# Kernel optimization log

Hardware: AMD Instinct MI355X
Metric: run time of the kernel (lower is better)

## Reference

```python
import jax, jax.numpy as jnp
import numpy as np

N_HEAD = 16


def setup_inputs() -> dict:
    key = jax.random.key(0)
    ks = jax.random.split(key, 4)
    B, T, C = 4, 2048, 1024
    x = jax.random.normal(ks[0], (B, T, C), dtype=jnp.float32)
    w_qkv = jax.random.normal(ks[1], (C, 3 * C), dtype=jnp.float32) * (1.0 / np.sqrt(C))
    b_qkv = jnp.zeros((3 * C,), dtype=jnp.float32)
    w_out = jax.random.normal(ks[2], (C, C), dtype=jnp.float32) * (1.0 / np.sqrt(C))
    b_out = jnp.zeros((C,), dtype=jnp.float32)
    return {"x": x, "w_qkv": w_qkv, "b_qkv": b_qkv, "w_out": w_out, "b_out": b_out}


def reference(x, w_qkv, b_qkv, w_out, b_out):
    B, T, C = x.shape
    H = N_HEAD
    D = C // H  # head_dim
    qkv = x @ w_qkv + b_qkv                      # [B,T,3C]
    q, k, v = jnp.split(qkv, 3, axis=-1)
    # [B,T,C] -> [B,H,T,D]
    q = q.reshape(B, T, H, D).transpose(0, 2, 1, 3)
    k = k.reshape(B, T, H, D).transpose(0, 2, 1, 3)
    v = v.reshape(B, T, H, D).transpose(0, 2, 1, 3)
    scores = jnp.einsum('bhqd,bhkd->bhqk', q, k) / jnp.sqrt(jnp.float32(D))
    causal = jnp.tril(jnp.ones((T, T), dtype=bool))
    scores = jnp.where(causal, scores, jnp.float32(-jnp.inf))
    attn = jax.nn.softmax(scores, axis=-1)       # dropout omitted (eval, p=0)
    out = jnp.einsum('bhqk,bhkd->bhqd', attn, v)
    out = out.transpose(0, 2, 1, 3).reshape(B, T, C)
    out = out @ w_out + b_out
    return out
```

## Files before the change

kernel.cpp:

```cpp
#include <hip/hip_runtime.h>
#include <hip/hip_bf16.h>

typedef unsigned short u16;
typedef unsigned int u32;
typedef __attribute__((ext_vector_type(8))) __bf16 bhalf8;
typedef __attribute__((ext_vector_type(8))) u16 us8;
typedef __attribute__((ext_vector_type(4))) u16 us4;
typedef __attribute__((ext_vector_type(4))) float f32x4;

#if __has_builtin(__builtin_amdgcn_mfma_f32_16x16x16_bf16)
typedef __attribute__((ext_vector_type(4))) __bf16 bhalf4;
#define MFMA16(a, b, c) __builtin_amdgcn_mfma_f32_16x16x16_bf16(a, b, c, 0, 0, 0)
#else
typedef __attribute__((ext_vector_type(4))) short bhalf4;
#define MFMA16(a, b, c) __builtin_amdgcn_mfma_f32_16x16x16bf16_1k(a, b, c, 0, 0, 0)
#endif

#if __has_builtin(__builtin_amdgcn_exp2f)
#define EXP2(x) __builtin_amdgcn_exp2f(x)
#else
#define EXP2(x) exp2f(x)
#endif

__device__ __forceinline__ u16 bf16rne(float f) {
  u32 u = __float_as_uint(f);
  u += 0x7FFFu + ((u >> 16) & 1u);
  return (u16)(u >> 16);
}

__device__ __forceinline__ u32 pkbf(float a, float b) {
  union { __hip_bfloat162 h; u32 w; } u;
  u.h = __float22bfloat162_rn(make_float2(a, b));
  return u.w;
}

__global__ __launch_bounds__(256) void cast4_kernel(const float* __restrict__ in,
                                                    u16* __restrict__ out, int n) {
  int i = (blockIdx.x * 256 + threadIdx.x) * 4;
  if (i >= n) return;
  float4 f = *(const float4*)(in + i);
  u32 lo = pkbf(f.x, f.y);
  u32 hi = pkbf(f.z, f.w);
  *(uint2*)(out + i) = make_uint2(lo, hi);
}

__global__ __launch_bounds__(256) void transpose_cast_kernel(const float* __restrict__ in,
                                                             u16* __restrict__ out,
                                                             int R, int Cn) {
  __shared__ float tile[32][33];
  int c0 = blockIdx.x * 32, r0 = blockIdx.y * 32;
  int tx = threadIdx.x, ty = threadIdx.y;
#pragma unroll
  for (int j = 0; j < 4; ++j)
    tile[ty + j * 8][tx] = in[(size_t)(r0 + ty + j * 8) * Cn + c0 + tx];
  __syncthreads();
#pragma unroll
  for (int j = 0; j < 4; ++j)
    out[(size_t)(c0 + ty + j * 8) * R + r0 + tx] = bf16rne(tile[tx][ty + j * 8]);
}

template <int MODE>
__global__ __launch_bounds__(256, 2) void gemm_bt_kernel(
    const u16* __restrict__ A, const u16* __restrict__ Bt, const float* __restrict__ bias,
    float* __restrict__ outf, u16* __restrict__ qb, u16* __restrict__ kb, u16* __restrict__ vb,
    int Mdim, int Ndim, int Kdim) {
  __shared__ __align__(16) u16 lA[128 * 64];
  __shared__ __align__(16) u16 lB[128 * 64];
  const int tid = threadIdx.x;
  const int lane = tid & 63;
  const int col = lane & 15, quad = lane >> 4;
  const int wid = tid >> 6;
  const int gx = (MODE == 0) ? 24 : 8;
  int id = blockIdx.y * gx + blockIdx.x;
  int g = id & 7, j = id >> 3;
  int vy = g * 8 + j / gx;
  int vx = j % gx;
  const int m0 = vy * 128, n0 = vx * 128;
  const int wm = (wid >> 1) * 64, wn = (wid & 1) * 64;
  const float QSC = 0.18033688011112042f;

  f32x4 acc[4][4];
#pragma unroll
  for (int i = 0; i < 4; ++i)
#pragma unroll
    for (int j2 = 0; j2 < 4; ++j2) acc[i][j2] = f32x4{0.f, 0.f, 0.f, 0.f};

  for (int k0 = 0; k0 < Kdim; k0 += 64) {
    const u16* Ag = A + (size_t)m0 * Kdim + k0;
    const u16* Bg = Bt + (size_t)n0 * Kdim + k0;
#pragma unroll
    for (int r = 0; r < 4; ++r) {
      int c = r * 256 + tid;
      int row = c >> 3;
      int bblk = (c & 7) ^ (row & 7);
      size_t ldsoff = (size_t)(r * 256 + (tid & 0xC0)) * 8;
      __builtin_amdgcn_global_load_lds(
          (const __attribute__((address_space(1))) void*)(Ag + (size_t)row * Kdim + bblk * 8),
          (__attribute__((address_space(3))) void*)(lA + ldsoff), 16, 0, 0);
      __builtin_amdgcn_global_load_lds(
          (const __attribute__((address_space(1))) void*)(Bg + (size_t)row * Kdim + bblk * 8),
          (__attribute__((address_space(3))) void*)(lB + ldsoff), 16, 0, 0);
    }
    __syncthreads();
#pragma unroll
    for (int ks = 0; ks < 2; ++ks) {
      bhalf8 af[4], bfr[4];
#pragma unroll
      for (int i = 0; i < 4; ++i) {
        int ra = wm + i * 16 + col;
        int rb = wn + i * 16 + col;
        af[i]  = *(const bhalf8*)&lA[ra * 64 + (((ks * 4 + quad) ^ (ra & 7)) * 8)];
        bfr[i] = *(const bhalf8*)&lB[rb * 64 + (((ks * 4 + quad) ^ (rb & 7)) * 8)];
      }
#pragma unroll
      for (int mt = 0; mt < 4; ++mt)
#pragma unroll
        for (int nt = 0; nt < 4; ++nt)
          acc[mt][nt] = __builtin_amdgcn_mfma_f32_16x16x32_bf16(af[mt], bfr[nt], acc[mt][nt], 0, 0, 0);
    }
    __syncthreads();
  }

  if (MODE == 0) {
#pragma unroll
    for (int nt = 0; nt < 4; ++nt) {
      int n = n0 + wn + nt * 16 + col;
      float bv = bias[n];
      int which = n >> 10, cc = n & 1023, hh = cc >> 6, dd = cc & 63;
      if (which == 2) {
#pragma unroll
        for (int mt = 0; mt < 4; ++mt) {
          int t0 = m0 + wm + mt * 16 + quad * 4;
          int bb = t0 >> 11, tt = t0 & 2047;
          us4 w;
#pragma unroll
          for (int reg = 0; reg < 4; ++reg) w[reg] = bf16rne(acc[mt][nt][reg] + bv);
          *(us4*)(vb + ((size_t)(bb * 16 + hh) * 64 + dd) * 2048 + tt) = w;
        }
      } else {
        u16* dst = which ? kb : qb;
        float sc = which ? 1.0f : QSC;
#pragma unroll
        for (int mt = 0; mt < 4; ++mt)
#pragma unroll
          for (int reg = 0; reg < 4; ++reg) {
            int m = m0 + wm + mt * 16 + quad * 4 + reg;
            int bb = m >> 11, tt = m & 2047;
            dst[((size_t)(bb * 16 + hh) * 2048 + tt) * 64 + dd] = bf16rne((acc[mt][nt][reg] + bv) * sc);
          }
      }
    }
  } else {
#pragma unroll
    for (int mt = 0; mt < 4; ++mt)
#pragma unroll
      for (int nt = 0; nt < 4; ++nt) {
        int n = n0 + wn + nt * 16 + col;
        float bv = bias[n];
#pragma unroll
        for (int reg = 0; reg < 4; ++reg) {
          int m = m0 + wm + mt * 16 + quad * 4 + reg;
          outf[(size_t)m * Ndim + n] = acc[mt][nt][reg] + bv;
        }
      }
  }
}

__global__ __launch_bounds__(256, 2) void attn_kernel(const u16* __restrict__ Q,
                                                      const u16* __restrict__ K,
                                                      const u16* __restrict__ VT,
                                                      u16* __restrict__ aout) {
  __shared__ __align__(16) u16 lK[2][128 * 64];
  __shared__ __align__(16) u16 lV[2][64 * 128];
  const int tid = threadIdx.x;
  const int lane = tid & 63, wid = tid >> 6;
  const int col = lane & 15, quad = lane >> 4;
  int id = blockIdx.y * 8 + blockIdx.x;
  int g = id & 7, j = id >> 3;
  const int bh = g * 8 + (j >> 3);
  const int bx = j & 7;
  const int b = bh >> 4, h = bh & 15;
  const u16* Qb = Q + (size_t)bh * 2048 * 64;
  const u16* Kb = K + (size_t)bh * 2048 * 64;
  const u16* Vb = VT + (size_t)bh * 64 * 2048;
  const int qbase = wid * 32;
  const int wuni = (tid & 0xC0);

  for (int phase = 0; phase < 2; ++phase) {
    const int qt = (phase == 0) ? (15 - bx) : bx;

    auto stage = [&](int kt, int bufi) {
      const u16* Kg = Kb + (size_t)kt * 128 * 64;
      const u16* Vg = Vb + (size_t)kt * 128;
#pragma unroll
      for (int r = 0; r < 4; ++r) {
        int c = r * 256 + tid;
        size_t ldsoff = (size_t)(r * 256 + wuni) * 8;
        int krow = c >> 3, kblk = (c & 7) ^ (krow & 7);
        __builtin_amdgcn_global_load_lds(
            (const __attribute__((address_space(1))) void*)(Kg + (size_t)krow * 64 + kblk * 8),
            (__attribute__((address_space(3))) void*)(&lK[bufi][0] + ldsoff), 16, 0, 0);
        int vrow = c >> 4, vblk = (c & 15) ^ (vrow & 15);
        __builtin_amdgcn_global_load_lds(
            (const __attribute__((address_space(1))) void*)(Vg + (size_t)vrow * 2048 + vblk * 8),
            (__attribute__((address_space(3))) void*)(&lV[bufi][0] + ldsoff), 16, 0, 0);
      }
    };

    bhalf8 qf[2][2];
#pragma unroll
    for (int ntq = 0; ntq < 2; ++ntq)
#pragma unroll
      for (int ks = 0; ks < 2; ++ks)
        qf[ntq][ks] = *(const bhalf8*)(Qb + (size_t)(qt * 128 + qbase + ntq * 16 + col) * 64 +
                                       ks * 32 + quad * 8);

    f32x4 oacc[4][2];
    float lr[2] = {0.f, 0.f};
#pragma unroll
    for (int dt = 0; dt < 4; ++dt)
#pragma unroll
      for (int ntq = 0; ntq < 2; ++ntq) oacc[dt][ntq] = f32x4{0.f, 0.f, 0.f, 0.f};

    stage(0, 0);

    for (int kt = 0; kt <= qt; ++kt) {
      const int cur = kt & 1;
      __syncthreads();
      if (kt < qt) stage(kt + 1, cur ^ 1);
      const bool diag = (kt == qt);
      const int ntkhi = diag ? (2 * wid + 2) : 8;

      f32x4 sacc[8][2];
#pragma unroll
      for (int ntk = 0; ntk < 8; ++ntk)
#pragma unroll
        for (int ntq = 0; ntq < 2; ++ntq) sacc[ntk][ntq] = f32x4{0.f, 0.f, 0.f, 0.f};
#pragma unroll
      for (int ks = 0; ks < 2; ++ks) {
        bhalf8 kf[8];
#pragma unroll
        for (int ntk = 0; ntk < 8; ++ntk)
          if (ntk < ntkhi) {
            int ra = ntk * 16 + col;
            kf[ntk] = *(const bhalf8*)&lK[cur][ra * 64 + (((ks * 4 + quad) ^ (ra & 7)) * 8)];
          }
#pragma unroll
        for (int ntk = 0; ntk < 8; ++ntk)
          if (ntk < ntkhi) {
#pragma unroll
            for (int ntq = 0; ntq < 2; ++ntq)
              sacc[ntk][ntq] = __builtin_amdgcn_mfma_f32_16x16x32_bf16(kf[ntk], qf[ntq][ks],
                                                                       sacc[ntk][ntq], 0, 0, 0);
          }
      }

      if (diag) {
#pragma unroll
        for (int ntk = 0; ntk < 8; ++ntk)
          if (ntk >= 2 * wid && ntk < 2 * wid + 2) {
#pragma unroll
            for (int ntq = 0; ntq < 2; ++ntq) {
              int qloc = qbase + ntq * 16 + col;
#pragma unroll
              for (int reg = 0; reg < 4; ++reg) {
                int kloc = ntk * 16 + quad * 4 + reg;
                if (kloc > qloc) sacc[ntk][ntq][reg] = -1e30f;
              }
            }
          }
      }

#pragma unroll
      for (int ntk = 0; ntk < 8; ++ntk)
        if (ntk < ntkhi) {
          bhalf4 vf[4];
#pragma unroll
          for (int dt = 0; dt < 4; ++dt) {
            int vrow = dt * 16 + col;
            vf[dt] = *(const bhalf4*)&lV[cur][vrow * 128 +
                                             (((ntk * 2 + (quad >> 1)) ^ col) * 8) + (quad & 1) * 4];
          }
#pragma unroll
          for (int ntq = 0; ntq < 2; ++ntq) {
            float p0 = EXP2(sacc[ntk][ntq][0]);
            float p1 = EXP2(sacc[ntk][ntq][1]);
            float p2 = EXP2(sacc[ntk][ntq][2]);
            float p3 = EXP2(sacc[ntk][ntq][3]);
            lr[ntq] += (p0 + p1) + (p2 + p3);
            union { u32 w[2]; bhalf4 v; } pfu;
            pfu.w[0] = pkbf(p0, p1);
            pfu.w[1] = pkbf(p2, p3);
#pragma unroll
            for (int dt = 0; dt < 4; ++dt)
              oacc[dt][ntq] = MFMA16(vf[dt], pfu.v, oacc[dt][ntq]);
          }
        }
    }

#pragma unroll
    for (int ntq = 0; ntq < 2; ++ntq) {
      float r = lr[ntq];
      r += __shfl_xor(r, 16);
      r += __shfl_xor(r, 32);
      float inv = 1.f / r;
      int q = qt * 128 + qbase + ntq * 16 + col;
      size_t base = ((size_t)(b * 2048 + q)) * 1024 + h * 64;
#pragma unroll
      for (int dt = 0; dt < 4; ++dt) {
        us4 w;
#pragma unroll
        for (int reg = 0; reg < 4; ++reg) w[reg] = bf16rne(oacc[dt][ntq][reg] * inv);
        *(us4*)(aout + base + dt * 16 + quad * 4) = w;
      }
    }
    __syncthreads();
  }
}

extern "C" void kernel_launch(void* const* d_in, const int* in_sizes, int n_in,
                              void* d_out, int out_size, void* d_ws, size_t ws_size,
                              hipStream_t stream) {
  const float* x     = (const float*)d_in[0];
  const float* w_qkv = (const float*)d_in[1];
  const float* b_qkv = (const float*)d_in[2];
  const float* w_out = (const float*)d_in[3];
  const float* b_out = (const float*)d_in[4];
  float* out = (float*)d_out;
  char* ws = (char*)d_ws;
  u16* xb    = (u16*)(ws);
  u16* wqkvT = (u16*)(ws + 16777216);
  u16* woutT = (u16*)(ws + 23068672);
  u16* qb    = (u16*)(ws + 25165824);
  u16* kb    = (u16*)(ws + 41943040);
  u16* vT    = (u16*)(ws + 58720256);
  u16* ab    = (u16*)(ws + 75497472);

  cast4_kernel<<<8192, 256, 0, stream>>>(x, xb, 8388608);
  dim3 tb(32, 8);
  transpose_cast_kernel<<<dim3(96, 32), tb, 0, stream>>>(w_qkv, wqkvT, 1024, 3072);
  transpose_cast_kernel<<<dim3(32, 32), tb, 0, stream>>>(w_out, woutT, 1024, 1024);
  gemm_bt_kernel<0><<<dim3(24, 64), 256, 0, stream>>>(xb, wqkvT, b_qkv, nullptr, qb, kb, vT,
                                                      8192, 3072, 1024);
  attn_kernel<<<dim3(8, 64), 256, 0, stream>>>(qb, kb, vT, ab);
  gemm_bt_kernel<1><<<dim3(8, 64), 256, 0, stream>>>(ab, woutT, b_out, out, nullptr, nullptr,
                                                     nullptr, 8192, 1024, 1024);
}
```

Measured before the change: 245.8 us.

## Shrink attention K/V tiles to 64 keys and merge prep kernels

```diff
diff --git a/kernel.cpp b/kernel.cpp
--- a/kernel.cpp
+++ b/kernel.cpp
@@ -34,22 +34,10 @@
   return u.w;
 }
 
-__global__ __launch_bounds__(256) void cast4_kernel(const float* __restrict__ in,
-                                                    u16* __restrict__ out, int n) {
-  int i = (blockIdx.x * 256 + threadIdx.x) * 4;
-  if (i >= n) return;
-  float4 f = *(const float4*)(in + i);
-  u32 lo = pkbf(f.x, f.y);
-  u32 hi = pkbf(f.z, f.w);
-  *(uint2*)(out + i) = make_uint2(lo, hi);
-}
-
-__global__ __launch_bounds__(256) void transpose_cast_kernel(const float* __restrict__ in,
-                                                             u16* __restrict__ out,
-                                                             int R, int Cn) {
+__device__ __forceinline__ void tcast_tile(const float* __restrict__ in, u16* __restrict__ out,
+                                           int R, int Cn, int c0, int r0, int tid) {
   __shared__ float tile[32][33];
-  int c0 = blockIdx.x * 32, r0 = blockIdx.y * 32;
-  int tx = threadIdx.x, ty = threadIdx.y;
+  int tx = tid & 31, ty = tid >> 5;
 #pragma unroll
   for (int j = 0; j < 4; ++j)
     tile[ty + j * 8][tx] = in[(size_t)(r0 + ty + j * 8) * Cn + c0 + tx];
@@ -57,6 +45,26 @@
 #pragma unroll
   for (int j = 0; j < 4; ++j)
     out[(size_t)(c0 + ty + j * 8) * R + r0 + tx] = bf16rne(tile[tx][ty + j * 8]);
+}
+
+__global__ __launch_bounds__(256) void prep_kernel(const float* __restrict__ x,
+                                                   const float* __restrict__ wqkv,
+                                                   const float* __restrict__ wout,
+                                                   u16* __restrict__ xb,
+                                                   u16* __restrict__ wqkvT,
+                                                   u16* __restrict__ woutT) {
+  int bid = blockIdx.x, tid = threadIdx.x;
+  if (bid < 8192) {
+    int i = (bid * 256 + tid) * 4;
+    float4 f = *(const float4*)(x + i);
+    *(uint2*)(xb + i) = make_uint2(pkbf(f.x, f.y), pkbf(f.z, f.w));
+  } else if (bid < 11264) {
+    int t = bid - 8192;
+    tcast_tile(wqkv, wqkvT, 1024, 3072, (t % 96) * 32, (t / 96) * 32, tid);
+  } else {
+    int t = bid - 11264;
+    tcast_tile(wout, woutT, 1024, 1024, (t % 32) * 32, (t / 32) * 32, tid);
+  }
 }
 
 template <int MODE>
@@ -166,12 +174,12 @@
   }
 }
 
-__global__ __launch_bounds__(256, 2) void attn_kernel(const u16* __restrict__ Q,
+__global__ __launch_bounds__(256, 4) void attn_kernel(const u16* __restrict__ Q,
                                                       const u16* __restrict__ K,
                                                       const u16* __restrict__ VT,
                                                       u16* __restrict__ aout) {
-  __shared__ __align__(16) u16 lK[2][128 * 64];
-  __shared__ __align__(16) u16 lV[2][64 * 128];
+  __shared__ __align__(16) u16 lK[2][64 * 64];
+  __shared__ __align__(16) u16 lV[2][64 * 64];
   const int tid = threadIdx.x;
   const int lane = tid & 63, wid = tid >> 6;
   const int col = lane & 15, quad = lane >> 4;
@@ -183,26 +191,31 @@
   const u16* Qb = Q + (size_t)bh * 2048 * 64;
   const u16* Kb = K + (size_t)bh * 2048 * 64;
   const u16* Vb = VT + (size_t)bh * 64 * 2048;
-  const int qbase = wid * 32;
-  const int wuni = (tid & 0xC0);
+  const int wuni = tid & 0xC0;
+
+  const int loffK0 = col * 64 + ((quad ^ (col & 7)) * 8);
+  const int loffK1 = col * 64 + (((4 + quad) ^ (col & 7)) * 8);
+  int loffV[4];
+#pragma unroll
+  for (int ntk = 0; ntk < 4; ++ntk)
+    loffV[ntk] = col * 64 + (((ntk * 2 + (quad >> 1)) ^ (col & 7)) * 8) + (quad & 1) * 4;
 
   for (int phase = 0; phase < 2; ++phase) {
     const int qt = (phase == 0) ? (15 - bx) : bx;
 
     auto stage = [&](int kt, int bufi) {
-      const u16* Kg = Kb + (size_t)kt * 128 * 64;
-      const u16* Vg = Vb + (size_t)kt * 128;
-#pragma unroll
-      for (int r = 0; r < 4; ++r) {
+      const u16* Kg = Kb + (size_t)kt * 64 * 64;
+      const u16* Vg = Vb + (size_t)kt * 64;
+#pragma unroll
+      for (int r = 0; r < 2; ++r) {
         int c = r * 256 + tid;
         size_t ldsoff = (size_t)(r * 256 + wuni) * 8;
-        int krow = c >> 3, kblk = (c & 7) ^ (krow & 7);
+        int row = c >> 3, blk = (c & 7) ^ (row & 7);
         __builtin_amdgcn_global_load_lds(
-            (const __attribute__((address_space(1))) void*)(Kg + (size_t)krow * 64 + kblk * 8),
+            (const __attribute__((address_space(1))) void*)(Kg + (size_t)row * 64 + blk * 8),
             (__attribute__((address_space(3))) void*)(&lK[bufi][0] + ldsoff), 16, 0, 0);
-        int vrow = c >> 4, vblk = (c & 15) ^ (vrow & 15);
         __builtin_amdgcn_global_load_lds(
-            (const __attribute__((address_space(1))) void*)(Vg + (size_t)vrow * 2048 + vblk * 8),
+            (const __attribute__((address_space(1))) void*)(Vg + (size_t)row * 2048 + blk * 8),
             (__attribute__((address_space(3))) void*)(&lV[bufi][0] + ldsoff), 16, 0, 0);
       }
     };
@@ -212,7 +225,7 @@
     for (int ntq = 0; ntq < 2; ++ntq)
 #pragma unroll
       for (int ks = 0; ks < 2; ++ks)
-        qf[ntq][ks] = *(const bhalf8*)(Qb + (size_t)(qt * 128 + qbase + ntq * 16 + col) * 64 +
+        qf[ntq][ks] = *(const bhalf8*)(Qb + (size_t)(qt * 128 + wid * 32 + ntq * 16 + col) * 64 +
                                        ks * 32 + quad * 8);
 
     f32x4 oacc[4][2];
@@ -222,65 +235,90 @@
 #pragma unroll
       for (int ntq = 0; ntq < 2; ++ntq) oacc[dt][ntq] = f32x4{0.f, 0.f, 0.f, 0.f};
 
-    stage(0, 0);
-
-    for (int kt = 0; kt <= qt; ++kt) {
-      const int cur = kt & 1;
-      __syncthreads();
-      if (kt < qt) stage(kt + 1, cur ^ 1);
-      const bool diag = (kt == qt);
-      const int ntkhi = diag ? (2 * wid + 2) : 8;
-
-      f32x4 sacc[8][2];
-#pragma unroll
-      for (int ntk = 0; ntk < 8; ++ntk)
+    auto compute_full = [&](const u16* Kbuf, const u16* Vbuf) {
+      f32x4 sacc[4][2];
+#pragma unroll
+      for (int ntk = 0; ntk < 4; ++ntk)
 #pragma unroll
         for (int ntq = 0; ntq < 2; ++ntq) sacc[ntk][ntq] = f32x4{0.f, 0.f, 0.f, 0.f};
 #pragma unroll
       for (int ks = 0; ks < 2; ++ks) {
-        bhalf8 kf[8];
-#pragma unroll
-        for (int ntk = 0; ntk < 8; ++ntk)
-          if (ntk < ntkhi) {
-            int ra = ntk * 16 + col;
-            kf[ntk] = *(const bhalf8*)&lK[cur][ra * 64 + (((ks * 4 + quad) ^ (ra & 7)) * 8)];
-          }
-#pragma unroll
-        for (int ntk = 0; ntk < 8; ++ntk)
-          if (ntk < ntkhi) {
+        const int lk = ks ? loffK1 : loffK0;
+        bhalf8 kf[4];
+#pragma unroll
+        for (int ntk = 0; ntk < 4; ++ntk) kf[ntk] = *(const bhalf8*)(Kbuf + lk + ntk * 1024);
+#pragma unroll
+        for (int ntk = 0; ntk < 4; ++ntk)
+#pragma unroll
+          for (int ntq = 0; ntq < 2; ++ntq)
+            sacc[ntk][ntq] = __builtin_amdgcn_mfma_f32_16x16x32_bf16(kf[ntk], qf[ntq][ks],
+                                                                     sacc[ntk][ntq], 0, 0, 0);
+      }
+#pragma unroll
+      for (int ntk = 0; ntk < 4; ++ntk) {
+        bhalf4 vf[4];
+#pragma unroll
+        for (int dt = 0; dt < 4; ++dt)
+          vf[dt] = *(const bhalf4*)(Vbuf + loffV[ntk] + dt * 1024);
+#pragma unroll
+        for (int ntq = 0; ntq < 2; ++ntq) {
+          float p0 = EXP2(sacc[ntk][ntq][0]);
+          float p1 = EXP2(sacc[ntk][ntq][1]);
+          float p2 = EXP2(sacc[ntk][ntq][2]);
+          float p3 = EXP2(sacc[ntk][ntq][3]);
+          lr[ntq] += (p0 + p1) + (p2 + p3);
+          union { u32 w[2]; bhalf4 v; } pfu;
+          pfu.w[0] = pkbf(p0, p1);
+          pfu.w[1] = pkbf(p2, p3);
+#pragma unroll
+          for (int dt = 0; dt < 4; ++dt)
+            oacc[dt][ntq] = MFMA16(vf[dt], pfu.v, oacc[dt][ntq]);
+        }
+      }
+    };
+
+    auto compute_diag = [&](const u16* Kbuf, const u16* Vbuf, int kbase) {
+      const int ntkhi = (wid & 1) ? 4 : 2;
+      const int ntklo = (wid & 1) * 2;
+      f32x4 sacc[4][2];
+#pragma unroll
+      for (int ntk = 0; ntk < 4; ++ntk)
+#pragma unroll
+        for (int ntq = 0; ntq < 2; ++ntq) sacc[ntk][ntq] = f32x4{0.f, 0.f, 0.f, 0.f};
+#pragma unroll
+      for (int ks = 0; ks < 2; ++ks) {
+        const int lk = ks ? loffK1 : loffK0;
+        bhalf8 kf[4];
+#pragma unroll
+        for (int ntk = 0; ntk < 4; ++ntk)
+          if (ntk < ntkhi) kf[ntk] = *(const bhalf8*)(Kbuf + lk + ntk * 1024);
+#pragma unroll
+        for (int ntk = 0; ntk < 4; ++ntk)
+          if (ntk < ntkhi)
 #pragma unroll
             for (int ntq = 0; ntq < 2; ++ntq)
               sacc[ntk][ntq] = __builtin_amdgcn_mfma_f32_16x16x32_bf16(kf[ntk], qf[ntq][ks],
                                                                        sacc[ntk][ntq], 0, 0, 0);
-          }
-      }
-
-      if (diag) {
-#pragma unroll
-        for (int ntk = 0; ntk < 8; ++ntk)
-          if (ntk >= 2 * wid && ntk < 2 * wid + 2) {
-#pragma unroll
-            for (int ntq = 0; ntq < 2; ++ntq) {
-              int qloc = qbase + ntq * 16 + col;
-#pragma unroll
-              for (int reg = 0; reg < 4; ++reg) {
-                int kloc = ntk * 16 + quad * 4 + reg;
-                if (kloc > qloc) sacc[ntk][ntq][reg] = -1e30f;
-              }
+      }
+#pragma unroll
+      for (int ntk = 0; ntk < 4; ++ntk)
+        if (ntk >= ntklo && ntk < ntkhi)
+#pragma unroll
+          for (int ntq = 0; ntq < 2; ++ntq) {
+            int qloc = wid * 32 + ntq * 16 + col;
+#pragma unroll
+            for (int reg = 0; reg < 4; ++reg) {
+              int kloc = kbase + ntk * 16 + quad * 4 + reg;
+              if (kloc > qloc) sacc[ntk][ntq][reg] = -1e30f;
             }
           }
-      }
-
-#pragma unroll
-      for (int ntk = 0; ntk < 8; ++ntk)
+#pragma unroll
+      for (int ntk = 0; ntk < 4; ++ntk)
         if (ntk < ntkhi) {
           bhalf4 vf[4];
 #pragma unroll
-          for (int dt = 0; dt < 4; ++dt) {
-            int vrow = dt * 16 + col;
-            vf[dt] = *(const bhalf4*)&lV[cur][vrow * 128 +
-                                             (((ntk * 2 + (quad >> 1)) ^ col) * 8) + (quad & 1) * 4];
-          }
+          for (int dt = 0; dt < 4; ++dt)
+            vf[dt] = *(const bhalf4*)(Vbuf + loffV[ntk] + dt * 1024);
 #pragma unroll
           for (int ntq = 0; ntq < 2; ++ntq) {
             float p0 = EXP2(sacc[ntk][ntq][0]);
@@ -296,7 +334,23 @@
               oacc[dt][ntq] = MFMA16(vf[dt], pfu.v, oacc[dt][ntq]);
           }
         }
-    }
+    };
+
+    stage(0, 0);
+    for (int p = 0; p < qt; ++p) {
+      __syncthreads();
+      stage(2 * p + 1, 1);
+      compute_full(&lK[0][0], &lV[0][0]);
+      __syncthreads();
+      stage(2 * p + 2, 0);
+      compute_full(&lK[1][0], &lV[1][0]);
+    }
+    __syncthreads();
+    stage(2 * qt + 1, 1);
+    if (wid >= 2) compute_full(&lK[0][0], &lV[0][0]);
+    else          compute_diag(&lK[0][0], &lV[0][0], 0);
+    __syncthreads();
+    if (wid >= 2) compute_diag(&lK[1][0], &lV[1][0], 64);
 
 #pragma unroll
     for (int ntq = 0; ntq < 2; ++ntq) {
@@ -304,7 +358,7 @@
       r += __shfl_xor(r, 16);
       r += __shfl_xor(r, 32);
       float inv = 1.f / r;
-      int q = qt * 128 + qbase + ntq * 16 + col;
+      int q = qt * 128 + wid * 32 + ntq * 16 + col;
       size_t base = ((size_t)(b * 2048 + q)) * 1024 + h * 64;
 #pragma unroll
       for (int dt = 0; dt < 4; ++dt) {
@@ -336,10 +390,7 @@
   u16* vT    = (u16*)(ws + 58720256);
   u16* ab    = (u16*)(ws + 75497472);
 
-  cast4_kernel<<<8192, 256, 0, stream>>>(x, xb, 8388608);
-  dim3 tb(32, 8);
-  transpose_cast_kernel<<<dim3(96, 32), tb, 0, stream>>>(w_qkv, wqkvT, 1024, 3072);
-  transpose_cast_kernel<<<dim3(32, 32), tb, 0, stream>>>(w_out, woutT, 1024, 1024);
+  prep_kernel<<<12288, 256, 0, stream>>>(x, w_qkv, w_out, xb, wqkvT, woutT);
   gemm_bt_kernel<0><<<dim3(24, 64), 256, 0, stream>>>(xb, wqkvT, b_qkv, nullptr, qb, kb, vT,
                                                       8192, 3072, 1024);
   attn_kernel<<<dim3(8, 64), 256, 0, stream>>>(qb, kb, vT, ab);
```

Result: slower. 348.4 us (+41.7%).
